# Optimization experiments

Measured on AMD Instinct MI355X. Metric: run time of the kernel, lower is better.

Reference implementation:

```python
import jax, jax.numpy as jnp
import numpy as np
from jax import lax

B, T, F, H, NSTEPS = 512, 512, 64, 128, 8
HALF = H // 2
LN_EPS = 1e-5


def gru_cell(x, h, w_ih, w_hh, b_ih, b_hh):
    # PyTorch GRUCell math. x: (B, in), h: (B, H)
    gx = x @ w_ih.T + b_ih            # (B, 3H)
    gh = h @ w_hh.T + b_hh            # (B, 3H)
    rx, zx, nx = jnp.split(gx, 3, axis=-1)
    rh, zh, nh = jnp.split(gh, 3, axis=-1)
    r = jax.nn.sigmoid(rx + rh)
    z = jax.nn.sigmoid(zx + zh)
    n = jnp.tanh(nx + r * nh)
    return (1.0 - z) * n + z * h


def run_gru_layer(xs, h0, w_ih, w_hh, b_ih, b_hh):
    # xs: (T, B, in) -> (T, B, H), last hidden (B, H)
    def step(h, x_t):
        h = gru_cell(x_t, h, w_ih, w_hh, b_ih, b_hh)
        return h, h
    h_last, ys = lax.scan(step, h0, xs)
    return ys, h_last


def setup_inputs() -> dict:
    key = jax.random.key(0)
    ks = iter(jax.random.split(key, 64))
    s = 1.0 / np.sqrt(H)

    def p(shape):
        return jax.random.uniform(next(ks), shape, jnp.float32, -s, s)

    inp = {"x": jax.random.normal(next(ks), (B, T, F), jnp.float32)}
    # encoder: 3 GRU layers (layer 0 takes F features, layers 1-2 take H)
    for l, d_in in enumerate([F, H, H]):
        inp[f"e{l}w_ih"] = p((3 * H, d_in))
        inp[f"e{l}w_hh"] = p((3 * H, H))
        inp[f"e{l}b_ih"] = p((3 * H,))
        inp[f"e{l}b_hh"] = p((3 * H,))
    # additive (Bahdanau) attention
    inp["aWq"] = p((H, H)); inp["abq"] = p((H,))
    inp["aWk"] = p((H, H)); inp["abk"] = p((H,))
    inp["av"] = p((H,))
    # decoder GRU: input is cat([context, state]) -> 2H
    inp["dw_ih"] = p((3 * H, 2 * H)); inp["dw_hh"] = p((3 * H, H))
    inp["db_ih"] = p((3 * H,)); inp["db_hh"] = p((3 * H,))
    # head: LayerNorm -> Linear(H, H/2) -> ReLU -> Linear(H/2, 1)
    inp["lng"] = jnp.ones((H,), jnp.float32); inp["lnb"] = jnp.zeros((H,), jnp.float32)
    inp["w1"] = p((HALF, H)); inp["b1"] = p((HALF,))
    inp["w2"] = p((1, HALF)); inp["b2"] = p((1,))
    return inp


def reference(x,
              e0w_ih, e0w_hh, e0b_ih, e0b_hh,
              e1w_ih, e1w_hh, e1b_ih, e1b_hh,
              e2w_ih, e2w_hh, e2b_ih, e2b_hh,
              aWq, abq, aWk, abk, av,
              dw_ih, dw_hh, db_ih, db_hh,
              lng, lnb, w1, b1, w2, b2):
    b = x.shape[0]
    xs = jnp.transpose(x, (1, 0, 2))  # (T, B, F)
    h0 = jnp.zeros((b, H), x.dtype)
    # 3-layer encoder GRU (dropout is eval-mode no-op)
    ys, _ = run_gru_layer(xs, h0, e0w_ih, e0w_hh, e0b_ih, e0b_hh)
    ys, _ = run_gru_layer(ys, h0, e1w_ih, e1w_hh, e1b_ih, e1b_hh)
    ys, h_n = run_gru_layer(ys, h0, e2w_ih, e2w_hh, e2b_ih, e2b_hh)
    enc = jnp.transpose(ys, (1, 0, 2))  # (B, T, H)

    keys = enc @ aWk.T + abk  # precompute key projection once: (B, T, H)

    def dec_step(h, _):
        q = h @ aWq.T + abq                                   # (B, H)
        scores = jnp.einsum('bth,h->bt', jnp.tanh(keys + q[:, None, :]), av)
        w = jax.nn.softmax(scores, axis=-1)                   # (B, T)
        ctx = jnp.einsum('bt,bth->bh', w, enc)                # (B, H)
        h_new = gru_cell(jnp.concatenate([ctx, h], axis=-1), h,
                         dw_ih, dw_hh, db_ih, db_hh)
        mu = h_new.mean(-1, keepdims=True)
        var = ((h_new - mu) ** 2).mean(-1, keepdims=True)
        y = (h_new - mu) / jnp.sqrt(var + LN_EPS) * lng + lnb
        y = jax.nn.relu(y @ w1.T + b1)
        pred = y @ w2.T + b2                                  # (B, 1)
        return h_new, pred

    _, preds = lax.scan(dec_step, h_n, None, length=NSTEPS)   # (n_steps, B, 1)
    return jnp.transpose(preds, (1, 0, 2))                    # (B, n_steps, 1)
```

## Files before the change

kernel.cpp:

```cpp
#include <hip/hip_runtime.h>
#include <hip/hip_bf16.h>
#include <cstdint>
#include <cstddef>

#define T_LEN 512
#define B_SZ  512
#define F_IN  64
#define H_DIM 128
#define NSTEP 8

typedef __attribute__((ext_vector_type(8))) short short8;
typedef __attribute__((ext_vector_type(4))) float f32x4;

__device__ __forceinline__ float fsig(float x) { return 1.0f / (1.0f + __expf(-x)); }
__device__ __forceinline__ float ftanh(float x) {
  float e = __expf(-2.0f * fabsf(x));
  float t = (1.0f - e) / (1.0f + e);
  return copysignf(t, x);
}
__device__ __forceinline__ unsigned short bf16hi(float x) {
  __hip_bfloat16 h = __float2bfloat16(x);
  return *(unsigned short*)&h;
}
__device__ __forceinline__ float bf2f(unsigned short u) {
  return __uint_as_float(((unsigned)u) << 16);
}
__device__ __forceinline__ float bflo(unsigned u) { return __uint_as_float(u << 16); }
__device__ __forceinline__ float bfhi(unsigned u) { return __uint_as_float(u & 0xffff0000u); }

template <int CTRL>
__device__ __forceinline__ float dpp_add(float v) {
  int p = __builtin_amdgcn_update_dpp(0, __float_as_int(v), CTRL, 0xF, 0xF, true);
  return v + __int_as_float(p);
}
__device__ __forceinline__ float row_sum16(float v) {
  v = dpp_add<0xB1>(v);
  v = dpp_add<0x4E>(v);
  v = dpp_add<0x124>(v);
  v = dpp_add<0x128>(v);
  return v;
}

__device__ __forceinline__ void split8(const float* p, short8& hi, short8& lo) {
  #pragma unroll
  for (int i = 0; i < 8; ++i) {
    const float v = p[i];
    const unsigned short h = bf16hi(v);
    hi[i] = (short)h;
    lo[i] = (short)bf16hi(v - bf2f(h));
  }
}

__device__ __forceinline__ void split_f4pair(const float4 a, const float4 b,
                                             short8& hi, short8& lo) {
  const float v[8] = {a.x, a.y, a.z, a.w, b.x, b.y, b.z, b.w};
  #pragma unroll
  for (int j = 0; j < 8; ++j) {
    const unsigned short h = bf16hi(v[j]);
    hi[j] = (short)h;
    lo[j] = (short)bf16hi(v[j] - bf2f(h));
  }
}

__global__ __launch_bounds__(256) void prep_split(
    const float* __restrict__ w0, const float* __restrict__ w1,
    const float* __restrict__ w2,
    unsigned short* __restrict__ hi, unsigned short* __restrict__ lo)
{
  const int i = blockIdx.x * 256 + threadIdx.x;
  if (i >= 122880) return;
  float v = (i < 24576) ? w0[i] : ((i < 73728) ? w1[i - 24576] : w2[i - 73728]);
  const unsigned short h = bf16hi(v);
  hi[i] = h;
  lo[i] = bf16hi(v - bf2f(h));
}

template <int IS_L0>
__global__ __launch_bounds__(512, 2) void rec_fused(
    const float* x,
    const unsigned short* Xhi,
    const unsigned short* Xlo,
    const unsigned short* __restrict__ Wih_hi,
    const unsigned short* __restrict__ Wih_lo,
    const float* __restrict__ w_hh, const float* __restrict__ b_ih,
    const float* __restrict__ b_hh,
    unsigned short* Hhi, unsigned short* Hlo)
{
  constexpr int KD   = IS_L0 ? 64 : 128;
  constexpr int NCK  = KD / 32;
  constexpr int WROW = KD * 2;
  constexpr int WGRAN = WROW / 16;
  constexpr int XBUF = IS_L0 ? 4096 : 8192;

  __shared__ unsigned short Wlds[384 * KD];
  __shared__ float gxlds[8 * 2 * 384];
  __shared__ unsigned short hbh[2][2048], hbl[2][2048];
  __shared__ unsigned short hsh[2][256], hsl[2][256];
  __shared__ __align__(16) unsigned char Xraw[2][XBUF];

  const int tid  = threadIdx.x;
  const int wv   = tid >> 6, lane = tid & 63;
  const int quad = lane >> 4, l16 = lane & 15;
  const int b0   = blockIdx.x * 2;
  const int c    = wv * 16 + l16;

  {
    unsigned char* wb = (unsigned char*)Wlds;
    #pragma unroll
    for (int k = 0; k < (384 * WGRAN) / 512; ++k) {
      const int idx = k * 512 + tid;
      const int row = idx / WGRAN;
      const int gg  = idx % WGRAN;
      const uint4 v = *(const uint4*)&Wih_hi[(size_t)row * KD + gg * 8];
      *(uint4*)&wb[row * WROW + ((gg ^ (row & 7)) * 16)] = v;
    }
  }

  short8 Wl_[3][NCK];
  #pragma unroll
  for (int g_ = 0; g_ < 3; ++g_)
    #pragma unroll
    for (int ck = 0; ck < NCK; ++ck)
      Wl_[g_][ck] = *(const short8*)&Wih_lo[(size_t)(g_ * 128 + c) * KD + ck * 32 + quad * 8];

  short8 Bh[3][4], Bl[3][4];
  #pragma unroll
  for (int g_ = 0; g_ < 3; ++g_)
    #pragma unroll
    for (int ck = 0; ck < 4; ++ck)
      split8(&w_hh[(size_t)(g_ * 128 + c) * 128 + ck * 32 + quad * 8],
             Bh[g_][ck], Bl[g_][ck]);

  float bias_r = 0.f, bias_z = 0.f, bihn = 0.f, bhhn = 0.f, h0 = 0.f, h1 = 0.f;
  if (quad == 0) {
    bias_r = b_ih[c] + b_hh[c];
    bias_z = b_ih[c + 128] + b_hh[c + 128];
    bihn = b_ih[c + 256];
    bhhn = b_hh[c + 256];
    hsh[0][c] = 0; hsh[0][128 + c] = 0;
    hsl[0][c] = 0; hsl[0][128 + c] = 0;
  }

  const int t8 = tid & 255;
  const int sr = t8 >> 4;
  const int sg = tid & 15;
  uint4 xr = {0, 0, 0, 0};

  auto load_xr = [&](int tgn) {
    if constexpr (IS_L0) {
      if (tid < 256)
        xr = *(const uint4*)&x[((size_t)(b0 + (sr & 1)) * T_LEN + tgn + (sr >> 1)) * 64 + sg * 4];
    } else {
      const unsigned short* src = (tid < 256) ? Xhi : Xlo;
      xr = *(const uint4*)&src[((size_t)(tgn + (sr >> 1)) * B_SZ + b0 + (sr & 1)) * 128 + sg * 8];
    }
  };
  auto store_xr = [&](int buf) {
    unsigned char* dstb = &Xraw[buf][0];
    const int off = sr * 256 + ((sg ^ (sr & 7)) * 16);
    if constexpr (IS_L0) {
      if (tid < 256) *(uint4*)&dstb[off] = xr;
    } else {
      *(uint4*)&dstb[(tid < 256 ? 0 : 4096) + off] = xr;
    }
  };
  auto flush_h = [&](int buf, int tp) {
    const int ft = t8 >> 5, fr = (t8 >> 4) & 1, fs = t8 & 15;
    const size_t go = ((size_t)(tp + ft) * B_SZ + b0 + fr) * 128 + fs * 8;
    const int lo_ = (ft * 2 + fr) * 128 + fs * 8;
    if (tid < 256) *(uint4*)&Hhi[go] = *(const uint4*)&hbh[buf][lo_];
    else           *(uint4*)&Hlo[go] = *(const uint4*)&hbl[buf][lo_];
  };

  load_xr(0);
  store_xr(0);
  load_xr(8);
  __syncthreads();

  for (int g = 0; g < 64; ++g) {
    if (g > 0) flush_h((g - 1) & 1, g * 8 - 8);

    short8 Xhf[NCK], Xlf[NCK];
    {
      const unsigned char* xbuf = &Xraw[g & 1][0];
      if constexpr (IS_L0) {
        #pragma unroll
        for (int ck = 0; ck < 2; ++ck) {
          const int g0 = ck * 8 + quad * 2;
          const float4 f0 = *(const float4*)&xbuf[l16 * 256 + ((g0 ^ (l16 & 7)) * 16)];
          const float4 f1 = *(const float4*)&xbuf[l16 * 256 + (((g0 + 1) ^ (l16 & 7)) * 16)];
          split_f4pair(f0, f1, Xhf[ck], Xlf[ck]);
        }
      } else {
        #pragma unroll
        for (int ck = 0; ck < 4; ++ck) {
          const int go = ((ck * 4 + quad) ^ (l16 & 7)) * 16;
          Xhf[ck] = *(const short8*)&xbuf[l16 * 256 + go];
          Xlf[ck] = *(const short8*)&xbuf[4096 + l16 * 256 + go];
        }
      }
    }
    {
      f32x4 ax[3][2];
      #pragma unroll
      for (int g_ = 0; g_ < 3; ++g_) {
        ax[g_][0] = (f32x4){0.f, 0.f, 0.f, 0.f};
        ax[g_][1] = (f32x4){0.f, 0.f, 0.f, 0.f};
      }
      const unsigned char* wb = (const unsigned char*)Wlds;
      #pragma unroll
      for (int ck = 0; ck < NCK; ++ck) {
        const int p = (NCK == 4) ? (ck >> 1) : ck;
        #pragma unroll
        for (int g_ = 0; g_ < 3; ++g_) {
          const int n = g_ * 128 + c;
          const short8 wh = *(const short8*)&wb[n * WROW + (((ck * 4 + quad) ^ (n & 7)) * 16)];
          ax[g_][p] = __builtin_amdgcn_mfma_f32_16x16x32_bf16(Xhf[ck], wh, ax[g_][p], 0, 0, 0);
          ax[g_][p] = __builtin_amdgcn_mfma_f32_16x16x32_bf16(Xhf[ck], Wl_[g_][ck], ax[g_][p], 0, 0, 0);
          ax[g_][p] = __builtin_amdgcn_mfma_f32_16x16x32_bf16(Xlf[ck], wh, ax[g_][p], 0, 0, 0);
        }
      }
      #pragma unroll
      for (int g_ = 0; g_ < 3; ++g_)
        #pragma unroll
        for (int reg = 0; reg < 4; ++reg) {
          const int tt_ = quad * 2 + (reg >> 1);
          const int r_  = reg & 1;
          gxlds[(tt_ * 2 + r_) * 384 + g_ * 128 + c] = ax[g_][0][reg] + ax[g_][1][reg];
        }
    }
    __syncthreads();

    #pragma unroll
    for (int tt = 0; tt < 8; ++tt) {
      float gr0 = 0.f, gz0 = 0.f, gn0 = 0.f, gr1 = 0.f, gz1 = 0.f, gn1 = 0.f;
      if (quad == 0) {
        const float* gp = &gxlds[tt * 768 + c];
        gr0 = gp[0];   gz0 = gp[128]; gn0 = gp[256];
        gr1 = gp[384]; gz1 = gp[512]; gn1 = gp[640];
      }

      short8 Ahf[4], Alf[4];
      if (l16 < 2) {
        #pragma unroll
        for (int ck = 0; ck < 4; ++ck) {
          const int ad = l16 * 128 + ck * 32 + quad * 8;
          Ahf[ck] = *(const short8*)&hsh[tt & 1][ad];
          Alf[ck] = *(const short8*)&hsl[tt & 1][ad];
        }
      } else {
        #pragma unroll
        for (int ck = 0; ck < 4; ++ck) {
          Ahf[ck] = (short8){0, 0, 0, 0, 0, 0, 0, 0};
          Alf[ck] = (short8){0, 0, 0, 0, 0, 0, 0, 0};
        }
      }

      f32x4 acc[3][2];
      #pragma unroll
      for (int g_ = 0; g_ < 3; ++g_) {
        acc[g_][0] = (f32x4){0.f, 0.f, 0.f, 0.f};
        acc[g_][1] = (f32x4){0.f, 0.f, 0.f, 0.f};
      }
      #pragma unroll
      for (int ck = 0; ck < 4; ++ck) {
        const int p = ck >> 1;
        #pragma unroll
        for (int g_ = 0; g_ < 3; ++g_) {
          acc[g_][p] = __builtin_amdgcn_mfma_f32_16x16x32_bf16(Ahf[ck], Bh[g_][ck], acc[g_][p], 0, 0, 0);
          acc[g_][p] = __builtin_amdgcn_mfma_f32_16x16x32_bf16(Ahf[ck], Bl[g_][ck], acc[g_][p], 0, 0, 0);
          acc[g_][p] = __builtin_amdgcn_mfma_f32_16x16x32_bf16(Alf[ck], Bh[g_][ck], acc[g_][p], 0, 0, 0);
        }
      }

      if (quad == 0) {
        const float ghr0 = acc[0][0][0] + acc[0][1][0];
        const float ghr1 = acc[0][0][1] + acc[0][1][1];
        const float ghz0 = acc[1][0][0] + acc[1][1][0];
        const float ghz1 = acc[1][0][1] + acc[1][1][1];
        const float ghn0 = acc[2][0][0] + acc[2][1][0];
        const float ghn1 = acc[2][0][1] + acc[2][1][1];
        const float r0 = fsig(gr0 + ghr0 + bias_r);
        const float z0 = fsig(gz0 + ghz0 + bias_z);
        const float nv0 = ftanh(gn0 + bihn + r0 * (ghn0 + bhhn));
        const float hn0 = (1.0f - z0) * nv0 + z0 * h0;
        const float r1 = fsig(gr1 + ghr1 + bias_r);
        const float z1 = fsig(gz1 + ghz1 + bias_z);
        const float nv1 = ftanh(gn1 + bihn + r1 * (ghn1 + bhhn));
        const float hn1 = (1.0f - z1) * nv1 + z1 * h1;
        h0 = hn0; h1 = hn1;
        const int nb = (tt + 1) & 1;
        const unsigned short hh0 = bf16hi(hn0), hh1 = bf16hi(hn1);
        const unsigned short hl0 = bf16hi(hn0 - bf2f(hh0));
        const unsigned short hl1 = bf16hi(hn1 - bf2f(hh1));
        hsh[nb][c] = hh0;       hsh[nb][128 + c] = hh1;
        hsl[nb][c] = hl0;       hsl[nb][128 + c] = hl1;
        const int hb = (tt * 2) * 128 + c;
        hbh[g & 1][hb] = hh0;       hbh[g & 1][hb + 128] = hh1;
        hbl[g & 1][hb] = hl0;       hbl[g & 1][hb + 128] = hl1;
      }

      if (tt == 7 && g + 1 < 64) {
        store_xr((g + 1) & 1);
        if (g + 2 < 64) load_xr((g + 2) * 8);
      }
      __syncthreads();
    }
  }
  flush_h(1, 504);
}

__global__ __launch_bounds__(256) void keys_gemm(
    const unsigned short* __restrict__ Ahi, const unsigned short* __restrict__ Alo,
    const float* __restrict__ aWk, const float* __restrict__ abk,
    unsigned short* __restrict__ Khi)
{
  __shared__ unsigned short Ah[64 * 40], Al[64 * 40];
  __shared__ unsigned short Bh[128 * 136], Bl[128 * 136];
  const int tid  = threadIdx.x;
  const int wave = tid >> 6, lane = tid & 63;
  const int quad = lane >> 4, l16 = lane & 15;
  const size_t m0 = (size_t)blockIdx.x * 64;

  for (int i = tid; i < 16384; i += 256) {
    const float v = aWk[i];
    const unsigned short h = bf16hi(v);
    const int r = i >> 7, k = i & 127;
    Bh[r * 136 + k] = h;
    Bl[r * 136 + k] = bf16hi(v - bf2f(h));
  }

  f32x4 acc[8];
  #pragma unroll
  for (int i = 0; i < 8; ++i) acc[i] = (f32x4){0.f, 0.f, 0.f, 0.f};
  float bias[8];
  #pragma unroll
  for (int nt = 0; nt < 8; ++nt) bias[nt] = abk[nt * 16 + l16];

  const int r = tid >> 2, c8 = (tid & 3) * 8;
  for (int kc = 0; kc < 128; kc += 32) {
    __syncthreads();
    const size_t src = (m0 + r) * 128 + kc + c8;
    *(uint4*)&Ah[r * 40 + c8] = *(const uint4*)&Ahi[src];
    *(uint4*)&Al[r * 40 + c8] = *(const uint4*)&Alo[src];
    __syncthreads();
    const short8 a_hi = *(const short8*)&Ah[(wave * 16 + l16) * 40 + quad * 8];
    const short8 a_lo = *(const short8*)&Al[(wave * 16 + l16) * 40 + quad * 8];
    #pragma unroll
    for (int nt = 0; nt < 8; ++nt) {
      const short8 b_hi = *(const short8*)&Bh[(nt * 16 + l16) * 136 + kc + quad * 8];
      const short8 b_lo = *(const short8*)&Bl[(nt * 16 + l16) * 136 + kc + quad * 8];
      acc[nt] = __builtin_amdgcn_mfma_f32_16x16x32_bf16(a_hi, b_hi, acc[nt], 0, 0, 0);
      acc[nt] = __builtin_amdgcn_mfma_f32_16x16x32_bf16(a_hi, b_lo, acc[nt], 0, 0, 0);
      acc[nt] = __builtin_amdgcn_mfma_f32_16x16x32_bf16(a_lo, b_hi, acc[nt], 0, 0, 0);
    }
  }
  #pragma unroll
  for (int nt = 0; nt < 8; ++nt) {
    #pragma unroll
    for (int reg = 0; reg < 4; ++reg) {
      const size_t m = m0 + wave * 16 + quad * 4 + reg;
      const int n = nt * 16 + l16;
      Khi[m * 128 + n] = bf16hi(acc[nt][reg] + bias[nt]);
    }
  }
}

__global__ __launch_bounds__(512) void decoder(
    const unsigned short* __restrict__ Hhi, const unsigned short* __restrict__ Hlo,
    const unsigned short* __restrict__ Khi,
    const float* __restrict__ aWq, const float* __restrict__ abq,
    const float* __restrict__ av,
    const float* __restrict__ dwih, const float* __restrict__ dwhh,
    const float* __restrict__ dbih, const float* __restrict__ dbhh,
    const float* __restrict__ lng, const float* __restrict__ lnb,
    const float* __restrict__ w1, const float* __restrict__ b1,
    const float* __restrict__ w2, const float* __restrict__ b2,
    float* __restrict__ out)
{
  __shared__ float h_s[128], q_s[128], av_s[128], s_s[512], w_s[512];
  __shared__ float part[8][128], u_s[256], gx_s[384], gh_s[384], y_s[128];
  __shared__ float red[16];
  const int b = blockIdx.x, tid = threadIdx.x;
  const int wave = tid >> 6, lane = tid & 63;
  const int tslot = lane >> 4, ks = lane & 15;

  if (tid < 128) {
    const size_t base = ((size_t)(T_LEN - 1) * B_SZ + b) * 128 + tid;
    h_s[tid] = bf2f(Hhi[base]) + bf2f(Hlo[base]);
    av_s[tid] = av[tid];
  }
  __syncthreads();

  for (int step = 0; step < NSTEP; ++step) {
    if (tid < 128) {
      float acc = abq[tid];
      const float* wr = &aWq[(size_t)tid * 128];
      #pragma unroll 8
      for (int k4 = 0; k4 < 32; ++k4) {
        const float4 hv = *(const float4*)&h_s[k4 * 4];
        const float4 wv = *(const float4*)&wr[k4 * 4];
        acc += hv.x * wv.x + hv.y * wv.y + hv.z * wv.z + hv.w * wv.w;
      }
      q_s[tid] = acc;
    }
    __syncthreads();
    #pragma unroll 2
    for (int it = 0; it < 16; ++it) {
      const int t = it * 32 + wave * 4 + tslot;
      const size_t kb = ((size_t)t * B_SZ + b) * 128 + ks * 8;
      const uint4 uh = *(const uint4*)&Khi[kb];
      const float4 q0 = *(const float4*)&q_s[ks * 8];
      const float4 q1 = *(const float4*)&q_s[ks * 8 + 4];
      const float4 a0 = *(const float4*)&av_s[ks * 8];
      const float4 a1 = *(const float4*)&av_s[ks * 8 + 4];
      float acc = ftanh(bflo(uh.x) + q0.x) * a0.x + ftanh(bfhi(uh.x) + q0.y) * a0.y
                + ftanh(bflo(uh.y) + q0.z) * a0.z + ftanh(bfhi(uh.y) + q0.w) * a0.w
                + ftanh(bflo(uh.z) + q1.x) * a1.x + ftanh(bfhi(uh.z) + q1.y) * a1.y
                + ftanh(bflo(uh.w) + q1.z) * a1.z + ftanh(bfhi(uh.w) + q1.w) * a1.w;
      acc = row_sum16(acc);
      if (ks == 0) s_s[t] = acc;
    }
    __syncthreads();
    {
      const float sv = s_s[tid];
      float mx = sv;
      #pragma unroll
      for (int o = 32; o; o >>= 1) mx = fmaxf(mx, __shfl_xor(mx, o, 64));
      if (lane == 0) red[wave] = mx;
      __syncthreads();
      mx = red[0];
      #pragma unroll
      for (int i = 1; i < 8; ++i) mx = fmaxf(mx, red[i]);
      const float e = __expf(sv - mx);
      float sm = e;
      #pragma unroll
      for (int o = 32; o; o >>= 1) sm += __shfl_xor(sm, o, 64);
      if (lane == 0) red[8 + wave] = sm;
      __syncthreads();
      float tot = red[8];
      #pragma unroll
      for (int i = 1; i < 8; ++i) tot += red[8 + i];
      w_s[tid] = e / tot;
    }
    __syncthreads();
    {
      const int th = tid >> 6;
      const int c2 = (tid & 63) * 2;
      float acc0 = 0.0f, acc1 = 0.0f;
      #pragma unroll 4
      for (int q = 0; q < 64; ++q) {
        const int t = th * 64 + q;
        const unsigned u = *(const unsigned*)&Hhi[((size_t)t * B_SZ + b) * 128 + c2];
        const float wt = w_s[t];
        acc0 += wt * bflo(u);
        acc1 += wt * bfhi(u);
      }
      part[th][c2] = acc0;
      part[th][c2 + 1] = acc1;
    }
    __syncthreads();
    if (tid < 128) {
      float s = part[0][tid];
      #pragma unroll
      for (int i = 1; i < 8; ++i) s += part[i][tid];
      u_s[tid] = s;
      u_s[128 + tid] = h_s[tid];
    }
    __syncthreads();
    if (tid < 384) {
      const int j = tid;
      float gxv = dbih[j], ghv = dbhh[j];
      const float* wxr = &dwih[(size_t)j * 256];
      const float* whr = &dwhh[(size_t)j * 128];
      #pragma unroll 8
      for (int k4 = 0; k4 < 64; ++k4) {
        const float4 uv = *(const float4*)&u_s[k4 * 4];
        const float4 wv = *(const float4*)&wxr[k4 * 4];
        gxv += uv.x * wv.x + uv.y * wv.y + uv.z * wv.z + uv.w * wv.w;
      }
      #pragma unroll 8
      for (int k4 = 0; k4 < 32; ++k4) {
        const float4 hv = *(const float4*)&h_s[k4 * 4];
        const float4 wv = *(const float4*)&whr[k4 * 4];
        ghv += hv.x * wv.x + hv.y * wv.y + hv.z * wv.z + hv.w * wv.w;
      }
      gx_s[j] = gxv; gh_s[j] = ghv;
    }
    __syncthreads();
    if (tid < 128) {
      const float r = fsig(gx_s[tid] + gh_s[tid]);
      const float z = fsig(gx_s[128 + tid] + gh_s[128 + tid]);
      const float n = ftanh(gx_s[256 + tid] + r * gh_s[256 + tid]);
      const float hn = (1.0f - z) * n + z * h_s[tid];
      h_s[tid] = hn;
      float s1 = hn, s2 = hn * hn;
      #pragma unroll
      for (int o = 32; o; o >>= 1) { s1 += __shfl_xor(s1, o, 64); s2 += __shfl_xor(s2, o, 64); }
      if ((tid & 63) == 0) { red[tid >> 6] = s1; red[4 + (tid >> 6)] = s2; }
    }
    __syncthreads();
    if (tid < 128) {
      const float hn  = h_s[tid];
      const float mu  = (red[0] + red[1]) * (1.0f / 128.0f);
      const float var = (red[4] + red[5]) * (1.0f / 128.0f) - mu * mu;
      y_s[tid] = (hn - mu) / sqrtf(var + 1e-5f) * lng[tid] + lnb[tid];
    }
    __syncthreads();
    if (tid < 64) {
      float acc = b1[tid];
      const float* wr = &w1[(size_t)tid * 128];
      #pragma unroll 8
      for (int k4 = 0; k4 < 32; ++k4) {
        const float4 yv = *(const float4*)&y_s[k4 * 4];
        const float4 wv = *(const float4*)&wr[k4 * 4];
        acc += yv.x * wv.x + yv.y * wv.y + yv.z * wv.z + yv.w * wv.w;
      }
      acc = fmaxf(acc, 0.0f);
      float v = acc * w2[tid];
      #pragma unroll
      for (int o = 32; o; o >>= 1) v += __shfl_xor(v, o, 64);
      if (tid == 0) out[(size_t)b * NSTEP + step] = v + b2[0];
    }
    __syncthreads();
  }
}

extern "C" void kernel_launch(void* const* d_in, const int* in_sizes, int n_in,
                              void* d_out, int out_size, void* d_ws, size_t ws_size,
                              hipStream_t stream)
{
  (void)in_sizes; (void)n_in; (void)out_size; (void)ws_size;
  const float* x    = (const float*)d_in[0];
  const float* ewih[3] = {(const float*)d_in[1], (const float*)d_in[5], (const float*)d_in[9]};
  const float* ewhh[3] = {(const float*)d_in[2], (const float*)d_in[6], (const float*)d_in[10]};
  const float* ebih[3] = {(const float*)d_in[3], (const float*)d_in[7], (const float*)d_in[11]};
  const float* ebhh[3] = {(const float*)d_in[4], (const float*)d_in[8], (const float*)d_in[12]};
  const float* aWq  = (const float*)d_in[13];
  const float* abq  = (const float*)d_in[14];
  const float* aWk  = (const float*)d_in[15];
  const float* abk  = (const float*)d_in[16];
  const float* av   = (const float*)d_in[17];
  const float* dwih = (const float*)d_in[18];
  const float* dwhh = (const float*)d_in[19];
  const float* dbih = (const float*)d_in[20];
  const float* dbhh = (const float*)d_in[21];
  const float* lng  = (const float*)d_in[22];
  const float* lnb  = (const float*)d_in[23];
  const float* w1   = (const float*)d_in[24];
  const float* b1   = (const float*)d_in[25];
  const float* w2   = (const float*)d_in[26];
  const float* b2   = (const float*)d_in[27];

  const size_t HN = (size_t)T_LEN * B_SZ * H_DIM;
  unsigned short* Hhi = (unsigned short*)d_ws;
  unsigned short* Hlo = Hhi + HN;
  float* regionC = (float*)(Hlo + HN);
  unsigned short* Whi = (unsigned short*)(regionC + 25165824 + 65536);
  unsigned short* Wlo = Whi + 122880;
  unsigned short* Khi = (unsigned short*)regionC;

  prep_split<<<dim3(480), dim3(256), 0, stream>>>(ewih[0], ewih[1], ewih[2], Whi, Wlo);

  rec_fused<1><<<dim3(256), dim3(512), 0, stream>>>(
      x, nullptr, nullptr, Whi, Wlo,
      ewhh[0], ebih[0], ebhh[0], Hhi, Hlo);
  rec_fused<0><<<dim3(256), dim3(512), 0, stream>>>(
      nullptr, Hhi, Hlo, Whi + 24576, Wlo + 24576,
      ewhh[1], ebih[1], ebhh[1], Hhi, Hlo);
  rec_fused<0><<<dim3(256), dim3(512), 0, stream>>>(
      nullptr, Hhi, Hlo, Whi + 73728, Wlo + 73728,
      ewhh[2], ebih[2], ebhh[2], Hhi, Hlo);

  keys_gemm<<<dim3(4096), dim3(256), 0, stream>>>(Hhi, Hlo, aWk, abk, Khi);
  decoder<<<dim3(512), dim3(512), 0, stream>>>(
      Hhi, Hlo, Khi, aWq, abq, av, dwih, dwhh, dbih, dbhh,
      lng, lnb, w1, b1, w2, b2, (float*)d_out);
}
```

Before: 2.691 ms.

## Interleave next-chunk input projection into recurrent steps of fused GRU kernel

Splits the per-chunk input-projection MFMAs for the next group of 8 timesteps into slices spread across the 8 recurrent steps of the current group, double-buffering the gate-input LDS. Inputs are loaded straight from global memory into registers instead of staging through LDS, and hidden-state flushes are split into half-chunks. The full __syncthreads after each step is replaced by an lgkmcnt wait plus s_barrier, and launch bounds drop to one block per SIMD-pair to allow more registers. The aim is to hide the input GEMM and memory latency behind the latency-bound serial recurrence, at the cost of higher register pressure and lower occupancy.

Result: slower. 3.127 ms (+16.2%).

```diff
diff --git a/kernel.cpp b/kernel.cpp
--- a/kernel.cpp
+++ b/kernel.cpp
@@ -27,6 +27,12 @@
 }
 __device__ __forceinline__ float bflo(unsigned u) { return __uint_as_float(u << 16); }
 __device__ __forceinline__ float bfhi(unsigned u) { return __uint_as_float(u & 0xffff0000u); }
+
+__device__ __forceinline__ void step_barrier() {
+  asm volatile("s_waitcnt lgkmcnt(0)" ::: "memory");
+  __builtin_amdgcn_s_barrier();
+  asm volatile("" ::: "memory");
+}
 
 template <int CTRL>
 __device__ __forceinline__ float dpp_add(float v) {
@@ -76,7 +82,7 @@
 }
 
 template <int IS_L0>
-__global__ __launch_bounds__(512, 2) void rec_fused(
+__global__ __launch_bounds__(512, 1) void rec_fused(
     const float* x,
     const unsigned short* Xhi,
     const unsigned short* Xlo,
@@ -86,17 +92,15 @@
     const float* __restrict__ b_hh,
     unsigned short* Hhi, unsigned short* Hlo)
 {
-  constexpr int KD   = IS_L0 ? 64 : 128;
-  constexpr int NCK  = KD / 32;
-  constexpr int WROW = KD * 2;
+  constexpr int KD    = IS_L0 ? 64 : 128;
+  constexpr int NCK   = KD / 32;
+  constexpr int WROW  = KD * 2;
   constexpr int WGRAN = WROW / 16;
-  constexpr int XBUF = IS_L0 ? 4096 : 8192;
 
   __shared__ unsigned short Wlds[384 * KD];
-  __shared__ float gxlds[8 * 2 * 384];
-  __shared__ unsigned short hbh[2][2048], hbl[2][2048];
+  __shared__ float gxlds[2][6144];
+  __shared__ unsigned short hb_h[2048], hb_l[2048];
   __shared__ unsigned short hsh[2][256], hsl[2][256];
-  __shared__ __align__(16) unsigned char Xraw[2][XBUF];
 
   const int tid  = threadIdx.x;
   const int wv   = tid >> 6, lane = tid & 63;
@@ -115,13 +119,6 @@
       *(uint4*)&wb[row * WROW + ((gg ^ (row & 7)) * 16)] = v;
     }
   }
-
-  short8 Wl_[3][NCK];
-  #pragma unroll
-  for (int g_ = 0; g_ < 3; ++g_)
-    #pragma unroll
-    for (int ck = 0; ck < NCK; ++ck)
-      Wl_[g_][ck] = *(const short8*)&Wih_lo[(size_t)(g_ * 128 + c) * KD + ck * 32 + quad * 8];
 
   short8 Bh[3][4], Bl[3][4];
   #pragma unroll
@@ -141,136 +138,183 @@
     hsl[0][c] = 0; hsl[0][128 + c] = 0;
   }
 
-  const int t8 = tid & 255;
-  const int sr = t8 >> 4;
-  const int sg = tid & 15;
-  uint4 xr = {0, 0, 0, 0};
-
-  auto load_xr = [&](int tgn) {
-    if constexpr (IS_L0) {
-      if (tid < 256)
-        xr = *(const uint4*)&x[((size_t)(b0 + (sr & 1)) * T_LEN + tgn + (sr >> 1)) * 64 + sg * 4];
-    } else {
-      const unsigned short* src = (tid < 256) ? Xhi : Xlo;
-      xr = *(const uint4*)&src[((size_t)(tgn + (sr >> 1)) * B_SZ + b0 + (sr & 1)) * 128 + sg * 8];
+  const f32x4 z4 = (f32x4){0.f, 0.f, 0.f, 0.f};
+  f32x4 ax[3][2];
+  #pragma unroll
+  for (int g_ = 0; g_ < 3; ++g_) { ax[g_][0] = z4; ax[g_][1] = z4; }
+
+  uint4  xh[4], xl[4];
+  float4 xf[4];
+  short8 xhf2[2], xlf2[2];
+  short8 wloA[NCK], wloB[NCK];
+
+  auto load_x_pair = [&](int tgn, int ck0_) {
+    #pragma unroll
+    for (int d = 0; d < 2; ++d) {
+      const int ck = ck0_ + d;
+      const size_t base =
+          ((size_t)(tgn + (l16 >> 1)) * B_SZ + b0 + (l16 & 1)) * 128 + ck * 32 + quad * 8;
+      xh[ck] = *(const uint4*)&Xhi[base];
+      xl[ck] = *(const uint4*)&Xlo[base];
     }
   };
-  auto store_xr = [&](int buf) {
-    unsigned char* dstb = &Xraw[buf][0];
-    const int off = sr * 256 + ((sg ^ (sr & 7)) * 16);
-    if constexpr (IS_L0) {
-      if (tid < 256) *(uint4*)&dstb[off] = xr;
-    } else {
-      *(uint4*)&dstb[(tid < 256 ? 0 : 4096) + off] = xr;
-    }
+  auto load_xf_ck = [&](int tgn, int ck) {
+    const size_t base =
+        ((size_t)(b0 + (l16 & 1)) * T_LEN + tgn + (l16 >> 1)) * 64 + ck * 32 + quad * 8;
+    xf[ck * 2]     = *(const float4*)&x[base];
+    xf[ck * 2 + 1] = *(const float4*)&x[base + 4];
   };
-  auto flush_h = [&](int buf, int tp) {
-    const int ft = t8 >> 5, fr = (t8 >> 4) & 1, fs = t8 & 15;
-    const size_t go = ((size_t)(tp + ft) * B_SZ + b0 + fr) * 128 + fs * 8;
-    const int lo_ = (ft * 2 + fr) * 128 + fs * 8;
-    if (tid < 256) *(uint4*)&Hhi[go] = *(const uint4*)&hbh[buf][lo_];
-    else           *(uint4*)&Hlo[go] = *(const uint4*)&hbl[buf][lo_];
+  auto load_wlo = [&](int g_, short8* dst) {
+    #pragma unroll
+    for (int ck = 0; ck < NCK; ++ck)
+      dst[ck] = *(const short8*)&Wih_lo[(size_t)(g_ * 128 + c) * KD + ck * 32 + quad * 8];
   };
-
-  load_xr(0);
-  store_xr(0);
-  load_xr(8);
+  const unsigned char* wbase = (const unsigned char*)Wlds;
+  auto gx3 = [&](int g_, int ck, const short8 xhfv, const short8 xlfv, const short8 wlov) {
+    const int gran = (ck * 4 + quad) ^ (c & 7);
+    const short8 wh = *(const short8*)&wbase[(g_ * 128 + c) * WROW + gran * 16];
+    const int p = (NCK == 4) ? (ck >> 1) : ck;
+    ax[g_][p] = __builtin_amdgcn_mfma_f32_16x16x32_bf16(xhfv, wh,   ax[g_][p], 0, 0, 0);
+    ax[g_][p] = __builtin_amdgcn_mfma_f32_16x16x32_bf16(xhfv, wlov, ax[g_][p], 0, 0, 0);
+    ax[g_][p] = __builtin_amdgcn_mfma_f32_16x16x32_bf16(xlfv, wh,   ax[g_][p], 0, 0, 0);
+  };
+  auto gx_write = [&](int g_, float* dst) {
+    #pragma unroll
+    for (int reg = 0; reg < 4; ++reg) {
+      const int tt_ = quad * 2 + (reg >> 1), r_ = reg & 1;
+      dst[(tt_ * 2 + r_) * 384 + g_ * 128 + c] = ax[g_][0][reg] + ax[g_][1][reg];
+    }
+    ax[g_][0] = z4; ax[g_][1] = z4;
+  };
+  auto flush_half = [&](int half, int tp) {
+    const int t8 = tid & 255;
+    const int o  = t8 * 4;
+    const int tt_ = o >> 8, rem = o & 255;
+    const int r_ = rem >> 7, c_ = rem & 127;
+    const size_t go = ((size_t)(tp + tt_) * B_SZ + b0 + r_) * 128 + c_;
+    const int lo_ = half * 1024 + tt_ * 256 + r_ * 128 + c_;
+    if (tid < 256) *(uint2*)&Hhi[go] = *(const uint2*)&hb_h[lo_];
+    else           *(uint2*)&Hlo[go] = *(const uint2*)&hb_l[lo_];
+  };
+
+  if constexpr (IS_L0) { load_xf_ck(0, 0); load_xf_ck(0, 1); }
+  else { load_x_pair(0, 0); load_x_pair(0, 2); }
+  load_wlo(0, wloA);
+  load_wlo(1, wloB);
   __syncthreads();
 
+  if constexpr (IS_L0) {
+    split_f4pair(xf[0], xf[1], xhf2[0], xlf2[0]);
+    split_f4pair(xf[2], xf[3], xhf2[1], xlf2[1]);
+    gx3(0, 0, xhf2[0], xlf2[0], wloA[0]);
+    gx3(0, 1, xhf2[1], xlf2[1], wloA[1]);
+    load_wlo(2, wloA);
+    gx3(1, 0, xhf2[0], xlf2[0], wloB[0]);
+    gx3(1, 1, xhf2[1], xlf2[1], wloB[1]);
+    gx3(2, 0, xhf2[0], xlf2[0], wloA[0]);
+    gx3(2, 1, xhf2[1], xlf2[1], wloA[1]);
+  } else {
+    gx3(0, 0, *(const short8*)&xh[0], *(const short8*)&xl[0], wloA[0]);
+    gx3(0, 1, *(const short8*)&xh[1], *(const short8*)&xl[1], wloA[1]);
+    gx3(0, 2, *(const short8*)&xh[2], *(const short8*)&xl[2], wloA[2]);
+    gx3(0, 3, *(const short8*)&xh[3], *(const short8*)&xl[3], wloA[3]);
+    load_wlo(2, wloA);
+    gx3(1, 0, *(const short8*)&xh[0], *(const short8*)&xl[0], wloB[0]);
+    gx3(1, 1, *(const short8*)&xh[1], *(const short8*)&xl[1], wloB[1]);
+    gx3(1, 2, *(const short8*)&xh[2], *(const short8*)&xl[2], wloB[2]);
+    gx3(1, 3, *(const short8*)&xh[3], *(const short8*)&xl[3], wloB[3]);
+    gx3(2, 0, *(const short8*)&xh[0], *(const short8*)&xl[0], wloA[0]);
+    gx3(2, 1, *(const short8*)&xh[1], *(const short8*)&xl[1], wloA[1]);
+    gx3(2, 2, *(const short8*)&xh[2], *(const short8*)&xl[2], wloA[2]);
+    gx3(2, 3, *(const short8*)&xh[3], *(const short8*)&xl[3], wloA[3]);
+  }
+  gx_write(0, &gxlds[0][0]);
+  gx_write(1, &gxlds[0][0]);
+  gx_write(2, &gxlds[0][0]);
+  __syncthreads();
+
   for (int g = 0; g < 64; ++g) {
-    if (g > 0) flush_h((g - 1) & 1, g * 8 - 8);
-
-    short8 Xhf[NCK], Xlf[NCK];
-    {
-      const unsigned char* xbuf = &Xraw[g & 1][0];
-      if constexpr (IS_L0) {
+    const int gn = g + 1;
+    const bool live = (gn < 64);
+    const float* gxr = &gxlds[g & 1][0];
+    float* gxw = &gxlds[gn & 1][0];
+    #pragma unroll
+    for (int tt = 0; tt < 8; ++tt) {
+      if (tt == 0) {
+        if (g > 0) flush_half(1, g * 8 - 4);
+        if (live) {
+          if constexpr (IS_L0) load_xf_ck(gn * 8, 0);
+          else load_x_pair(gn * 8, 0);
+        }
+      }
+      if (tt == 1 && live) {
+        if constexpr (IS_L0) load_xf_ck(gn * 8, 1);
+        else load_x_pair(gn * 8, 2);
+        load_wlo(0, wloA);
+      }
+      if (tt == 3 && live) load_wlo(1, wloB);
+      if (tt == 4) flush_half(0, g * 8);
+      if (tt == 5 && live) load_wlo(2, wloA);
+
+      float gr0 = 0.f, gz0 = 0.f, gn0v = 0.f, gr1 = 0.f, gz1 = 0.f, gn1v = 0.f;
+      if (quad == 0) {
+        const float* gp = gxr + tt * 768 + c;
+        gr0 = gp[0];   gz0 = gp[128]; gn0v = gp[256];
+        gr1 = gp[384]; gz1 = gp[512]; gn1v = gp[640];
+      }
+
+      short8 Ahf[4], Alf[4];
+      #pragma unroll
+      for (int ck = 0; ck < 4; ++ck) {
+        const int ad = (l16 & 1) * 128 + ck * 32 + quad * 8;
+        Ahf[ck] = *(const short8*)&hsh[tt & 1][ad];
+        Alf[ck] = *(const short8*)&hsl[tt & 1][ad];
+      }
+
+      f32x4 acc[3][2];
+      #pragma unroll
+      for (int g_ = 0; g_ < 3; ++g_) {
         #pragma unroll
-        for (int ck = 0; ck < 2; ++ck) {
-          const int g0 = ck * 8 + quad * 2;
-          const float4 f0 = *(const float4*)&xbuf[l16 * 256 + ((g0 ^ (l16 & 7)) * 16)];
-          const float4 f1 = *(const float4*)&xbuf[l16 * 256 + (((g0 + 1) ^ (l16 & 7)) * 16)];
-          split_f4pair(f0, f1, Xhf[ck], Xlf[ck]);
+        for (int p = 0; p < 2; ++p) {
+          const int k0 = p * 2;
+          acc[g_][p] = __builtin_amdgcn_mfma_f32_16x16x32_bf16(Ahf[k0], Bh[g_][k0], z4, 0, 0, 0);
+          acc[g_][p] = __builtin_amdgcn_mfma_f32_16x16x32_bf16(Ahf[k0], Bl[g_][k0], acc[g_][p], 0, 0, 0);
+          acc[g_][p] = __builtin_amdgcn_mfma_f32_16x16x32_bf16(Alf[k0], Bh[g_][k0], acc[g_][p], 0, 0, 0);
+          acc[g_][p] = __builtin_amdgcn_mfma_f32_16x16x32_bf16(Ahf[k0+1], Bh[g_][k0+1], acc[g_][p], 0, 0, 0);
+          acc[g_][p] = __builtin_amdgcn_mfma_f32_16x16x32_bf16(Ahf[k0+1], Bl[g_][k0+1], acc[g_][p], 0, 0, 0);
+          acc[g_][p] = __builtin_amdgcn_mfma_f32_16x16x32_bf16(Alf[k0+1], Bh[g_][k0+1], acc[g_][p], 0, 0, 0);
         }
-      } else {
-        #pragma unroll
-        for (int ck = 0; ck < 4; ++ck) {
-          const int go = ((ck * 4 + quad) ^ (l16 & 7)) * 16;
-          Xhf[ck] = *(const short8*)&xbuf[l16 * 256 + go];
-          Xlf[ck] = *(const short8*)&xbuf[4096 + l16 * 256 + go];
+      }
+
+      if (live) {
+        if constexpr (IS_L0) {
+          if (tt == 1) split_f4pair(xf[0], xf[1], xhf2[0], xlf2[0]);
+          if (tt == 2) {
+            split_f4pair(xf[2], xf[3], xhf2[1], xlf2[1]);
+            gx3(0, 0, xhf2[0], xlf2[0], wloA[0]);
+            gx3(0, 1, xhf2[1], xlf2[1], wloA[1]);
+          }
+          if (tt == 4) { gx3(1, 0, xhf2[0], xlf2[0], wloB[0]);
+                         gx3(1, 1, xhf2[1], xlf2[1], wloB[1]); }
+          if (tt == 6) { gx3(2, 0, xhf2[0], xlf2[0], wloA[0]);
+                         gx3(2, 1, xhf2[1], xlf2[1], wloA[1]); }
+        } else {
+          if (tt == 2) { gx3(0, 0, *(const short8*)&xh[0], *(const short8*)&xl[0], wloA[0]);
+                         gx3(0, 1, *(const short8*)&xh[1], *(const short8*)&xl[1], wloA[1]); }
+          if (tt == 3) { gx3(0, 2, *(const short8*)&xh[2], *(const short8*)&xl[2], wloA[2]);
+                         gx3(0, 3, *(const short8*)&xh[3], *(const short8*)&xl[3], wloA[3]); }
+          if (tt == 4) { gx3(1, 0, *(const short8*)&xh[0], *(const short8*)&xl[0], wloB[0]);
+                         gx3(1, 1, *(const short8*)&xh[1], *(const short8*)&xl[1], wloB[1]); }
+          if (tt == 5) { gx3(1, 2, *(const short8*)&xh[2], *(const short8*)&xl[2], wloB[2]);
+                         gx3(1, 3, *(const short8*)&xh[3], *(const short8*)&xl[3], wloB[3]); }
+          if (tt == 6) { gx3(2, 0, *(const short8*)&xh[0], *(const short8*)&xl[0], wloA[0]);
+                         gx3(2, 1, *(const short8*)&xh[1], *(const short8*)&xl[1], wloA[1]); }
+          if (tt == 7) { gx3(2, 2, *(const short8*)&xh[2], *(const short8*)&xl[2], wloA[2]);
+                         gx3(2, 3, *(const short8*)&xh[3], *(const short8*)&xl[3], wloA[3]); }
         }
-      }
-    }
-    {
-      f32x4 ax[3][2];
-      #pragma unroll
-      for (int g_ = 0; g_ < 3; ++g_) {
-        ax[g_][0] = (f32x4){0.f, 0.f, 0.f, 0.f};
-        ax[g_][1] = (f32x4){0.f, 0.f, 0.f, 0.f};
-      }
-      const unsigned char* wb = (const unsigned char*)Wlds;
-      #pragma unroll
-      for (int ck = 0; ck < NCK; ++ck) {
-        const int p = (NCK == 4) ? (ck >> 1) : ck;
-        #pragma unroll
-        for (int g_ = 0; g_ < 3; ++g_) {
-          const int n = g_ * 128 + c;
-          const short8 wh = *(const short8*)&wb[n * WROW + (((ck * 4 + quad) ^ (n & 7)) * 16)];
-          ax[g_][p] = __builtin_amdgcn_mfma_f32_16x16x32_bf16(Xhf[ck], wh, ax[g_][p], 0, 0, 0);
-          ax[g_][p] = __builtin_amdgcn_mfma_f32_16x16x32_bf16(Xhf[ck], Wl_[g_][ck], ax[g_][p], 0, 0, 0);
-          ax[g_][p] = __builtin_amdgcn_mfma_f32_16x16x32_bf16(Xlf[ck], wh, ax[g_][p], 0, 0, 0);
-        }
-      }
-      #pragma unroll
-      for (int g_ = 0; g_ < 3; ++g_)
-        #pragma unroll
-        for (int reg = 0; reg < 4; ++reg) {
-          const int tt_ = quad * 2 + (reg >> 1);
-          const int r_  = reg & 1;
-          gxlds[(tt_ * 2 + r_) * 384 + g_ * 128 + c] = ax[g_][0][reg] + ax[g_][1][reg];
-        }
-    }
-    __syncthreads();
-
-    #pragma unroll
-    for (int tt = 0; tt < 8; ++tt) {
-      float gr0 = 0.f, gz0 = 0.f, gn0 = 0.f, gr1 = 0.f, gz1 = 0.f, gn1 = 0.f;
-      if (quad == 0) {
-        const float* gp = &gxlds[tt * 768 + c];
-        gr0 = gp[0];   gz0 = gp[128]; gn0 = gp[256];
-        gr1 = gp[384]; gz1 = gp[512]; gn1 = gp[640];
-      }
-
-      short8 Ahf[4], Alf[4];
-      if (l16 < 2) {
-        #pragma unroll
-        for (int ck = 0; ck < 4; ++ck) {
-          const int ad = l16 * 128 + ck * 32 + quad * 8;
-          Ahf[ck] = *(const short8*)&hsh[tt & 1][ad];
-          Alf[ck] = *(const short8*)&hsl[tt & 1][ad];
-        }
-      } else {
-        #pragma unroll
-        for (int ck = 0; ck < 4; ++ck) {
-          Ahf[ck] = (short8){0, 0, 0, 0, 0, 0, 0, 0};
-          Alf[ck] = (short8){0, 0, 0, 0, 0, 0, 0, 0};
-        }
-      }
-
-      f32x4 acc[3][2];
-      #pragma unroll
-      for (int g_ = 0; g_ < 3; ++g_) {
-        acc[g_][0] = (f32x4){0.f, 0.f, 0.f, 0.f};
-        acc[g_][1] = (f32x4){0.f, 0.f, 0.f, 0.f};
-      }
-      #pragma unroll
-      for (int ck = 0; ck < 4; ++ck) {
-        const int p = ck >> 1;
-        #pragma unroll
-        for (int g_ = 0; g_ < 3; ++g_) {
-          acc[g_][p] = __builtin_amdgcn_mfma_f32_16x16x32_bf16(Ahf[ck], Bh[g_][ck], acc[g_][p], 0, 0, 0);
-          acc[g_][p] = __builtin_amdgcn_mfma_f32_16x16x32_bf16(Ahf[ck], Bl[g_][ck], acc[g_][p], 0, 0, 0);
-          acc[g_][p] = __builtin_amdgcn_mfma_f32_16x16x32_bf16(Alf[ck], Bh[g_][ck], acc[g_][p], 0, 0, 0);
-        }
+        if (tt == 4) gx_write(0, gxw);
+        if (tt == 6) gx_write(1, gxw);
+        if (tt == 7) gx_write(2, gxw);
       }
 
       if (quad == 0) {
@@ -282,11 +326,11 @@
         const float ghn1 = acc[2][0][1] + acc[2][1][1];
         const float r0 = fsig(gr0 + ghr0 + bias_r);
         const float z0 = fsig(gz0 + ghz0 + bias_z);
-        const float nv0 = ftanh(gn0 + bihn + r0 * (ghn0 + bhhn));
+        const float nv0 = ftanh(gn0v + bihn + r0 * (ghn0 + bhhn));
         const float hn0 = (1.0f - z0) * nv0 + z0 * h0;
         const float r1 = fsig(gr1 + ghr1 + bias_r);
         const float z1 = fsig(gz1 + ghz1 + bias_z);
-        const float nv1 = ftanh(gn1 + bihn + r1 * (ghn1 + bhhn));
+        const float nv1 = ftanh(gn1v + bihn + r1 * (ghn1 + bhhn));
         const float hn1 = (1.0f - z1) * nv1 + z1 * h1;
         h0 = hn0; h1 = hn1;
         const int nb = (tt + 1) & 1;
@@ -295,19 +339,14 @@
         const unsigned short hl1 = bf16hi(hn1 - bf2f(hh1));
         hsh[nb][c] = hh0;       hsh[nb][128 + c] = hh1;
         hsl[nb][c] = hl0;       hsl[nb][128 + c] = hl1;
-        const int hb = (tt * 2) * 128 + c;
-        hbh[g & 1][hb] = hh0;       hbh[g & 1][hb + 128] = hh1;
-        hbl[g & 1][hb] = hl0;       hbl[g & 1][hb + 128] = hl1;
-      }
-
-      if (tt == 7 && g + 1 < 64) {
-        store_xr((g + 1) & 1);
-        if (g + 2 < 64) load_xr((g + 2) * 8);
-      }
-      __syncthreads();
-    }
-  }
-  flush_h(1, 504);
+        const int hb = (tt >> 2) * 1024 + (tt & 3) * 256 + c;
+        hb_h[hb] = hh0;       hb_h[hb + 128] = hh1;
+        hb_l[hb] = hl0;       hb_l[hb + 128] = hl1;
+      }
+      step_barrier();
+    }
+  }
+  flush_half(1, 508);
 }
 
 __global__ __launch_bounds__(256) void keys_gemm(
```
